# Kernel optimization log

Hardware: AMD Instinct MI355X
Metric: run time of the kernel (lower is better)

The kernel has to match this reference:

```python
import jax, jax.numpy as jnp
import numpy as np

ROPE_BASE = 10000.0

def _rope_tables(pos, d_head):
    # pos: (T,) int; returns cos,sin of shape (T, d_head//2)
    half = d_head // 2
    inv_freq = 1.0 / (ROPE_BASE ** (jnp.arange(half, dtype=jnp.float32) / half))
    ang = pos.astype(jnp.float32)[:, None] * inv_freq[None, :]
    return jnp.cos(ang), jnp.sin(ang)

def _apply_rope(x, cos, sin):
    # x: (B, H, T, D); cos/sin: (T, D//2); rotate-half convention
    x1, x2 = jnp.split(x, 2, axis=-1)
    c = cos[None, None, :, :]
    s = sin[None, None, :, :]
    return jnp.concatenate([x1 * c - x2 * s, x1 * s + x2 * c], axis=-1)

def setup_inputs() -> dict:
    key = jax.random.key(0)
    ks = jax.random.split(key, 8)
    B, T, C = 16, 4, 2048
    n_head, n_kv_head, d_head = 16, 4, 128
    S_cache = 4096
    sd = 1.0 / np.sqrt(C)
    return {
        "x": jax.random.normal(ks[0], (B, T, C), dtype=jnp.float32),
        "cache_k": jax.random.normal(ks[1], (B, n_kv_head, S_cache, d_head), dtype=jnp.float32),
        "cache_v": jax.random.normal(ks[2], (B, n_kv_head, S_cache, d_head), dtype=jnp.float32),
        "wq": jax.random.normal(ks[3], (C, n_head * d_head), dtype=jnp.float32) * sd,
        "wk": jax.random.normal(ks[4], (C, n_kv_head * d_head), dtype=jnp.float32) * sd,
        "wv": jax.random.normal(ks[5], (C, n_kv_head * d_head), dtype=jnp.float32) * sd,
        "w_proj": jax.random.normal(ks[6], (C, C), dtype=jnp.float32) * sd,
        "start_pos": 4096,
    }

def reference(x, cache_k, cache_v, wq, wk, wv, w_proj, start_pos):
    B, T, C = x.shape
    n_head, n_kv_head = 16, 4
    d_head = C // n_head
    group_size = n_head // n_kv_head
    sliding_window, sink = 2048, 4

    # projections -> (B, H, T, D)
    q = (x @ wq).reshape(B, T, n_head, d_head).transpose(0, 2, 1, 3)
    k = (x @ wk).reshape(B, T, n_kv_head, d_head).transpose(0, 2, 1, 3)
    v = (x @ wv).reshape(B, T, n_kv_head, d_head).transpose(0, 2, 1, 3)

    # RoPE at absolute positions [start_pos, start_pos+T)
    pos = jnp.arange(start_pos, start_pos + T)
    cos, sin = _rope_tables(pos, d_head)
    q = _apply_rope(q, cos, sin)
    k = _apply_rope(k, cos, sin)

    # KV cache concat along sequence dim
    k_all = jnp.concatenate([cache_k, k], axis=2)
    v_all = jnp.concatenate([cache_v, v], axis=2)

    # sliding window + attention sink slicing (4096+T > 2048+4)
    if k_all.shape[2] > sliding_window + sink:
        k_all = jnp.concatenate([k_all[:, :, :sink, :], k_all[:, :, -sliding_window:, :]], axis=2)
        v_all = jnp.concatenate([v_all[:, :, :sink, :], v_all[:, :, -sliding_window:, :]], axis=2)

    # GQA: expand KV heads to match query heads (repeat_interleave on head dim)
    k_attn = jnp.repeat(k_all, group_size, axis=1)
    v_attn = jnp.repeat(v_all, group_size, axis=1)

    # SDPA, is_causal=False (decode path with cache), dropout=0 (eval)
    scale = 1.0 / jnp.sqrt(jnp.float32(d_head))
    scores = jnp.einsum('bhtd,bhsd->bhts', q, k_attn) * scale
    attn = jax.nn.softmax(scores, axis=-1)
    y = jnp.einsum('bhts,bhsd->bhtd', attn, v_attn)

    y = y.transpose(0, 2, 1, 3).reshape(B, T, C)
    return y @ w_proj
```

## Files before the change

kernel.cpp:

```cpp
#include <hip/hip_runtime.h>
#include <math.h>

#define BB   16
#define TT   4
#define CC   2048
#define NH   16
#define NKV  4
#define DH   128
#define GRP  4
#define SCACHE 4096
#define SATT 2052
#define CS   128
#define NCH  17
#define KSPL 8

typedef unsigned int  uint32;
typedef unsigned short ushort_t;
typedef __attribute__((ext_vector_type(8))) __bf16 bf16x8;
typedef __attribute__((ext_vector_type(4))) float  f32x4;

__device__ __forceinline__ uint32 f2bf_bits(float f) {
    uint32 u = __float_as_uint(f);
    return (u + 0x7FFFu + ((u >> 16) & 1u)) >> 16;
}
__device__ __forceinline__ uint32 pk2(float lo, float hi) {
    return f2bf_bits(lo) | (f2bf_bits(hi) << 16);
}

#define Q_OFF    0
#define KNEW_OFF 524288
#define VNEW_OFF 655360
#define Y_OFF    786432
#define SCR_OFF  1310720

__global__ __launch_bounds__(256) void k_qkv(
    const float* __restrict__ x, const float* __restrict__ wq,
    const float* __restrict__ wk, const float* __restrict__ wv,
    float* __restrict__ part_qkv)
{
    __shared__ float xs[64][256];
    int ns = blockIdx.x, ks = blockIdx.y;
    int tid = threadIdx.x;
    int k0 = ks * 256;

    #pragma unroll
    for (int it = 0; it < 16; ++it) {
        int slot = it * 256 + tid;
        int row = slot >> 6, c4 = slot & 63;
        *(float4*)&xs[row][c4 * 4] = *(const float4*)(x + (size_t)row * CC + k0 + c4 * 4);
    }
    __syncthreads();

    int cp = tid & 31, rg = tid >> 5;
    const float* wp; int ldw, col;
    if (ns < 32)      { ldw = 2048; col = ns * 64 + cp * 2;
                        wp = wq + (size_t)k0 * 2048 + ns * 64 + cp * 2; }
    else if (ns < 40) { ldw = 512;  col = 2048 + (ns - 32) * 64 + cp * 2;
                        wp = wk + (size_t)k0 * 512 + (ns - 32) * 64 + cp * 2; }
    else              { ldw = 512;  col = 2560 + (ns - 40) * 64 + cp * 2;
                        wp = wv + (size_t)k0 * 512 + (ns - 40) * 64 + cp * 2; }

    float a[16];
    #pragma unroll
    for (int i = 0; i < 16; ++i) a[i] = 0.f;

    for (int k = 0; k < 256; k += 4) {
        float2 w0 = *(const float2*)(wp);
        float2 w1 = *(const float2*)(wp + ldw);
        float2 w2 = *(const float2*)(wp + 2 * ldw);
        float2 w3 = *(const float2*)(wp + 3 * ldw);
        wp += 4 * ldw;
        #pragma unroll
        for (int m = 0; m < 8; ++m) {
            float4 xv = *(const float4*)&xs[rg * 8 + m][k];
            float s0 = a[2*m], s1 = a[2*m+1];
            s0 = fmaf(xv.x, w0.x, s0); s1 = fmaf(xv.x, w0.y, s1);
            s0 = fmaf(xv.y, w1.x, s0); s1 = fmaf(xv.y, w1.y, s1);
            s0 = fmaf(xv.z, w2.x, s0); s1 = fmaf(xv.z, w2.y, s1);
            s0 = fmaf(xv.w, w3.x, s0); s1 = fmaf(xv.w, w3.y, s1);
            a[2*m] = s0; a[2*m+1] = s1;
        }
    }
    #pragma unroll
    for (int m = 0; m < 8; ++m)
        *(float2*)(part_qkv + ((size_t)(ks * 64 + rg * 8 + m) * 3072) + col) =
            make_float2(a[2*m], a[2*m+1]);
}

__global__ __launch_bounds__(256) void k_fix(
    const float* __restrict__ part_qkv, const int* __restrict__ spp,
    float* __restrict__ qws, float* __restrict__ knew, float* __restrict__ vnew)
{
    int u = blockIdx.x * 256 + threadIdx.x;
    int m = blockIdx.y;
    int b = m >> 2, t = m & 3;
    int sp = spp[0];
    const float NEG_L2_10K_64 = -0.20762050593048633f;

    if (u < 1024) {
        int h = u >> 6, d = u & 63;
        int col = h * 128 + d;
        float s1 = 0.f, s2 = 0.f;
        #pragma unroll
        for (int ks = 0; ks < KSPL; ++ks) {
            const float* p = part_qkv + (size_t)(ks * 64 + m) * 3072;
            s1 += p[col]; s2 += p[col + 64];
        }
        float inv = exp2f((float)d * NEG_L2_10K_64);
        float ang = (float)(sp + t) * inv;
        float cc = cosf(ang), ss = sinf(ang);
        float* dst = qws + (size_t)((b * NH + h) * TT + t) * DH + d;
        dst[0]  = s1 * cc - s2 * ss;
        dst[64] = s1 * ss + s2 * cc;
    } else if (u < 1280) {
        int v = u - 1024;
        int kv = v >> 6, d = v & 63;
        int col = 2048 + kv * 128 + d;
        float s1 = 0.f, s2 = 0.f;
        #pragma unroll
        for (int ks = 0; ks < KSPL; ++ks) {
            const float* p = part_qkv + (size_t)(ks * 64 + m) * 3072;
            s1 += p[col]; s2 += p[col + 64];
        }
        float inv = exp2f((float)d * NEG_L2_10K_64);
        float ang = (float)(sp + t) * inv;
        float cc = cosf(ang), ss = sinf(ang);
        float* dst = knew + (size_t)((b * NKV + kv) * TT + t) * DH + d;
        dst[0]  = s1 * cc - s2 * ss;
        dst[64] = s1 * ss + s2 * cc;
    } else {
        int v = u - 1280;
        int c0 = v * 2;
        int kv = c0 >> 7, dd = c0 & 127;
        float s1 = 0.f, s2 = 0.f;
        #pragma unroll
        for (int ks = 0; ks < KSPL; ++ks) {
            const float* p = part_qkv + (size_t)(ks * 64 + m) * 3072 + 2560 + c0;
            s1 += p[0]; s2 += p[1];
        }
        float* dst = vnew + (size_t)((b * NKV + kv) * TT + t) * DH + dd;
        dst[0] = s1; dst[1] = s2;
    }
}

__device__ __forceinline__ const float* kv_row(
    const float* cache, const float* newt, int bk, int j)
{
    if (j < 4)         return cache + ((size_t)bk * SCACHE + j) * DH;
    else if (j < 2048) return cache + ((size_t)bk * SCACHE + j + 2048) * DH;
    else               return newt  + ((size_t)(bk * TT + (j - 2048))) * DH;
}

__global__ __launch_bounds__(256) void k_attn(
    const float* __restrict__ qws,
    const float* __restrict__ kc, const float* __restrict__ vc,
    const float* __restrict__ knew, const float* __restrict__ vnew,
    float* __restrict__ part)
{
    __shared__ ushort_t kv_lds[128 * 136];
    __shared__ ushort_t p_lds[16 * 136];
    __shared__ float    red_a[64];
    __shared__ float    red_b[64];

    int bx = blockIdx.x;
    int c  = bx % NCH;
    int bk = bx / NCH;
    int b  = bk >> 2, kvh = bk & 3;
    int j0 = c * CS;
    int jn = (SATT - j0 < CS) ? (SATT - j0) : CS;
    int tid  = threadIdx.x;
    int wave = tid >> 6, lane = tid & 63;
    int quad = lane >> 4, l15 = lane & 15;
    const float scale = 0.08838834764831845f;

    bf16x8 aq[4];
    {
        int h = kvh * GRP + (l15 >> 2), t = l15 & 3;
        const float* qr = qws + (size_t)((b * NH + h) * TT + t) * DH;
        #pragma unroll
        for (int ks = 0; ks < 4; ++ks) {
            const float* s = qr + ks * 32 + quad * 8;
            float4 f0 = *(const float4*)s;
            float4 f1 = *(const float4*)(s + 4);
            union { uint32 u[4]; bf16x8 v; } pk;
            pk.u[0] = pk2(f0.x, f0.y); pk.u[1] = pk2(f0.z, f0.w);
            pk.u[2] = pk2(f1.x, f1.y); pk.u[3] = pk2(f1.z, f1.w);
            aq[ks] = pk.v;
        }
    }

    {
        float4 kf[16];
        #pragma unroll
        for (int it = 0; it < 8; ++it) {
            int slot = it * 256 + tid;
            int row = slot >> 4, d0 = (slot & 15) * 8;
            const float* kr = kv_row(kc, knew, bk, j0 + (row < jn ? row : 0)) + d0;
            kf[2*it]   = *(const float4*)kr;
            kf[2*it+1] = *(const float4*)(kr + 4);
        }
        #pragma unroll
        for (int it = 0; it < 8; ++it) {
            int slot = it * 256 + tid;
            int row = slot >> 4, d0 = (slot & 15) * 8;
            union { uint32 u[4]; bf16x8 v; } pk;
            pk.u[0] = pk.u[1] = pk.u[2] = pk.u[3] = 0;
            if (row < jn) {
                pk.u[0] = pk2(kf[2*it].x, kf[2*it].y);
                pk.u[1] = pk2(kf[2*it].z, kf[2*it].w);
                pk.u[2] = pk2(kf[2*it+1].x, kf[2*it+1].y);
                pk.u[3] = pk2(kf[2*it+1].z, kf[2*it+1].w);
            }
            *(bf16x8*)&kv_lds[row * 136 + d0] = pk.v;
        }
    }
    __syncthreads();

    int n0 = wave * 32;
    f32x4 s0 = {0.f, 0.f, 0.f, 0.f}, s1 = {0.f, 0.f, 0.f, 0.f};
    #pragma unroll
    for (int ks = 0; ks < 4; ++ks) {
        bf16x8 b0 = *(const bf16x8*)&kv_lds[(n0 + l15) * 136 + ks * 32 + quad * 8];
        bf16x8 b1 = *(const bf16x8*)&kv_lds[(n0 + 16 + l15) * 136 + ks * 32 + quad * 8];
        s0 = __builtin_amdgcn_mfma_f32_16x16x32_bf16(aq[ks], b0, s0, 0, 0, 0);
        s1 = __builtin_amdgcn_mfma_f32_16x16x32_bf16(aq[ks], b1, s1, 0, 0, 0);
    }

    float4 va[8], vb[8];
    int key0 = 2 * lane;
    bool okA = key0 < jn, okB = key0 + 1 < jn;
    {
        const float* ra = kv_row(vc, vnew, bk, j0 + (okA ? key0 : 0));
        const float* rb = kv_row(vc, vnew, bk, j0 + (okB ? key0 + 1 : 0));
        #pragma unroll
        for (int i = 0; i < 8; ++i) {
            int d = wave * 32 + i * 4;
            va[i] = *(const float4*)(ra + d);
            vb[i] = *(const float4*)(rb + d);
        }
    }

    int c0 = n0 + l15, c1 = n0 + 16 + l15;
    bool v0ok = c0 < jn, v1ok = c1 < jn;
    float sc0[4], sc1[4];
    #pragma unroll
    for (int i = 0; i < 4; ++i) {
        sc0[i] = v0ok ? s0[i] * scale : -1e30f;
        sc1[i] = v1ok ? s1[i] * scale : -1e30f;
        float v = fmaxf(sc0[i], sc1[i]);
        v = fmaxf(v, __shfl_xor(v, 1));
        v = fmaxf(v, __shfl_xor(v, 2));
        v = fmaxf(v, __shfl_xor(v, 4));
        v = fmaxf(v, __shfl_xor(v, 8));
        if (l15 == 0) red_a[wave * 16 + quad * 4 + i] = v;
    }
    __syncthreads();

    #pragma unroll
    for (int i = 0; i < 4; ++i) {
        int r = quad * 4 + i;
        float M = fmaxf(fmaxf(red_a[r], red_a[16 + r]),
                        fmaxf(red_a[32 + r], red_a[48 + r]));
        float p0 = __expf(sc0[i] - M);
        float p1 = __expf(sc1[i] - M);
        p_lds[r * 136 + c0] = (ushort_t)f2bf_bits(p0);
        p_lds[r * 136 + c1] = (ushort_t)f2bf_bits(p1);
        float v = p0 + p1;
        v += __shfl_xor(v, 1);
        v += __shfl_xor(v, 2);
        v += __shfl_xor(v, 4);
        v += __shfl_xor(v, 8);
        if (l15 == 0) red_b[wave * 16 + r] = v;
    }

    {
        uint32* vt32 = (uint32*)kv_lds;
        #pragma unroll
        for (int i = 0; i < 8; ++i) {
            int d = wave * 32 + i * 4;
            float4 fa = okA ? va[i] : make_float4(0.f, 0.f, 0.f, 0.f);
            float4 fb = okB ? vb[i] : make_float4(0.f, 0.f, 0.f, 0.f);
            vt32[(d + 0) * 68 + lane] = pk2(fa.x, fb.x);
            vt32[(d + 1) * 68 + lane] = pk2(fa.y, fb.y);
            vt32[(d + 2) * 68 + lane] = pk2(fa.z, fb.z);
            vt32[(d + 3) * 68 + lane] = pk2(fa.w, fb.w);
        }
    }
    __syncthreads();

    if (tid < 16) {
        int r = tid;
        float M = fmaxf(fmaxf(red_a[r], red_a[16 + r]),
                        fmaxf(red_a[32 + r], red_a[48 + r]));
        float L = red_b[r] + red_b[16 + r] + red_b[32 + r] + red_b[48 + r];
        float* rp = part + ((size_t)(bk * NCH + c) * 16 + r) * 132;
        rp[0] = M; rp[1] = L;
    }

    int d0 = wave * 32;
    f32x4 o0 = {0.f, 0.f, 0.f, 0.f}, o1 = {0.f, 0.f, 0.f, 0.f};
    #pragma unroll
    for (int ks = 0; ks < 4; ++ks) {
        bf16x8 ap = *(const bf16x8*)&p_lds[l15 * 136 + ks * 32 + quad * 8];
        bf16x8 b0 = *(const bf16x8*)&kv_lds[(d0 + l15) * 136 + ks * 32 + quad * 8];
        bf16x8 b1 = *(const bf16x8*)&kv_lds[(d0 + 16 + l15) * 136 + ks * 32 + quad * 8];
        o0 = __builtin_amdgcn_mfma_f32_16x16x32_bf16(ap, b0, o0, 0, 0, 0);
        o1 = __builtin_amdgcn_mfma_f32_16x16x32_bf16(ap, b1, o1, 0, 0, 0);
    }
    float* dstb = part + (size_t)(bk * NCH + c) * 16 * 132;
    #pragma unroll
    for (int i = 0; i < 4; ++i) {
        int row = quad * 4 + i;
        dstb[row * 132 + 4 + d0 + l15]      = o0[i];
        dstb[row * 132 + 4 + d0 + 16 + l15] = o1[i];
    }
}

__global__ __launch_bounds__(128) void k_comb(
    const float* __restrict__ part, float* __restrict__ yws)
{
    int bx = blockIdx.x;
    int t = bx & 3, h = (bx >> 2) & 15, b = bx >> 6;
    int bk = b * NKV + (h >> 2);
    int r  = (h & 3) * 4 + t;
    int d  = threadIdx.x;
    float M = -1e30f;
    for (int c = 0; c < NCH; ++c)
        M = fmaxf(M, part[((size_t)(bk * NCH + c) * 16 + r) * 132]);
    float L = 0.f, y = 0.f;
    for (int c = 0; c < NCH; ++c) {
        const float* pp = part + ((size_t)(bk * NCH + c) * 16 + r) * 132;
        float w = __expf(pp[0] - M);
        L += w * pp[1];
        y  = fmaf(w, pp[4 + d], y);
    }
    yws[(size_t)(b * TT + t) * CC + h * DH + d] = y / L;
}

__global__ __launch_bounds__(256) void k_proj(
    const float* __restrict__ yws, const float* __restrict__ wp,
    float* __restrict__ part_p)
{
    __shared__ float xs[64][256];
    int ns = blockIdx.x, ks = blockIdx.y;
    int tid = threadIdx.x;
    int k0 = ks * 256;
    #pragma unroll
    for (int it = 0; it < 16; ++it) {
        int slot = it * 256 + tid;
        int row = slot >> 6, c4 = slot & 63;
        *(float4*)&xs[row][c4 * 4] = *(const float4*)(yws + (size_t)row * CC + k0 + c4 * 4);
    }
    __syncthreads();

    int cp = tid & 31, rg = tid >> 5;
    int n = ns * 64 + cp * 2;
    const float* w = wp + (size_t)k0 * CC + n;
    float a[16];
    #pragma unroll
    for (int i = 0; i < 16; ++i) a[i] = 0.f;

    for (int k = 0; k < 256; k += 4) {
        float2 w0 = *(const float2*)(w);
        float2 w1 = *(const float2*)(w + CC);
        float2 w2 = *(const float2*)(w + 2 * CC);
        float2 w3 = *(const float2*)(w + 3 * CC);
        w += 4 * CC;
        #pragma unroll
        for (int m = 0; m < 8; ++m) {
            float4 xv = *(const float4*)&xs[rg * 8 + m][k];
            float s0 = a[2*m], s1 = a[2*m+1];
            s0 = fmaf(xv.x, w0.x, s0); s1 = fmaf(xv.x, w0.y, s1);
            s0 = fmaf(xv.y, w1.x, s0); s1 = fmaf(xv.y, w1.y, s1);
            s0 = fmaf(xv.z, w2.x, s0); s1 = fmaf(xv.z, w2.y, s1);
            s0 = fmaf(xv.w, w3.x, s0); s1 = fmaf(xv.w, w3.y, s1);
            a[2*m] = s0; a[2*m+1] = s1;
        }
    }
    #pragma unroll
    for (int m = 0; m < 8; ++m)
        *(float2*)(part_p + ((size_t)(ks * 64 + rg * 8 + m) * CC) + n) =
            make_float2(a[2*m], a[2*m+1]);
}

__global__ __launch_bounds__(256) void k_out(
    const float* __restrict__ part_p, float* __restrict__ out)
{
    int gt = blockIdx.x * 256 + threadIdx.x;
    float s = 0.f;
    #pragma unroll
    for (int ks = 0; ks < KSPL; ++ks) s += part_p[(size_t)ks * 64 * CC + gt];
    out[gt] = s;
}

extern "C" void kernel_launch(void* const* d_in, const int* in_sizes, int n_in,
                              void* d_out, int out_size, void* d_ws, size_t ws_size,
                              hipStream_t stream)
{
    const float* x   = (const float*)d_in[0];
    const float* ck  = (const float*)d_in[1];
    const float* cv  = (const float*)d_in[2];
    const float* wq  = (const float*)d_in[3];
    const float* wk  = (const float*)d_in[4];
    const float* wv  = (const float*)d_in[5];
    const float* wpj = (const float*)d_in[6];
    const int*   sp  = (const int*)d_in[7];
    char* ws = (char*)d_ws;
    float* qws  = (float*)(ws + Q_OFF);
    float* knew = (float*)(ws + KNEW_OFF);
    float* vnew = (float*)(ws + VNEW_OFF);
    float* yws  = (float*)(ws + Y_OFF);
    float* scr  = (float*)(ws + SCR_OFF);
    float* out  = (float*)d_out;

    hipLaunchKernelGGL(k_qkv,  dim3(48, 8),   dim3(256), 0, stream, x, wq, wk, wv, scr);
    hipLaunchKernelGGL(k_fix,  dim3(6, 64),   dim3(256), 0, stream, scr, sp, qws, knew, vnew);
    hipLaunchKernelGGL(k_attn, dim3(64 * NCH), dim3(256), 0, stream, qws, ck, cv, knew, vnew, scr);
    hipLaunchKernelGGL(k_comb, dim3(1024),    dim3(128), 0, stream, scr, yws);
    hipLaunchKernelGGL(k_proj, dim3(32, 8),   dim3(256), 0, stream, yws, wpj, scr);
    hipLaunchKernelGGL(k_out,  dim3(512),     dim3(256), 0, stream, scr, out);
}
```

Baseline: 361.7 us.

## Load K directly into MFMA registers, skip LDS staging, and prefetch V early

The attention kernel now loads each wave's K rows straight from global memory into registers in the MFMA B-operand layout. This removes the shared-memory staging pass for K and one block-wide barrier. V loads are issued at kernel start and split into two halves, so part of the V transpose into LDS overlaps the score MFMAs and softmax. This should cut latency and synchronisation in a memory-bound kernel, at the cost of more live registers and less regular K load patterns.

```diff
diff --git a/kernel.cpp b/kernel.cpp
--- a/kernel.cpp
+++ b/kernel.cpp
@@ -157,7 +157,7 @@
     const float* __restrict__ knew, const float* __restrict__ vnew,
     float* __restrict__ part)
 {
-    __shared__ ushort_t kv_lds[128 * 136];
+    __shared__ ushort_t vt_lds[128 * 136];
     __shared__ ushort_t p_lds[16 * 136];
     __shared__ float    red_a[64];
     __shared__ float    red_b[64];
@@ -173,6 +173,34 @@
     int quad = lane >> 4, l15 = lane & 15;
     const float scale = 0.08838834764831845f;
 
+    int n0 = wave * 32;
+
+    int rA = n0 + l15, rB = n0 + 16 + l15;
+    const float* kA = kv_row(kc, knew, bk, j0 + (rA < jn ? rA : 0));
+    const float* kB = kv_row(kc, knew, bk, j0 + (rB < jn ? rB : 0));
+    float4 ka[8], kb[8];
+    #pragma unroll
+    for (int ks = 0; ks < 4; ++ks) {
+        const float* pa = kA + ks * 32 + quad * 8;
+        const float* pb = kB + ks * 32 + quad * 8;
+        ka[2*ks]   = *(const float4*)pa;
+        ka[2*ks+1] = *(const float4*)(pa + 4);
+        kb[2*ks]   = *(const float4*)pb;
+        kb[2*ks+1] = *(const float4*)(pb + 4);
+    }
+
+    int key0 = 2 * lane;
+    bool okA = key0 < jn, okB = key0 + 1 < jn;
+    const float* rva = kv_row(vc, vnew, bk, j0 + (okA ? key0 : 0));
+    const float* rvb = kv_row(vc, vnew, bk, j0 + (okB ? key0 + 1 : 0));
+    float4 va0[4], vb0[4];
+    #pragma unroll
+    for (int i = 0; i < 4; ++i) {
+        int d = n0 + i * 4;
+        va0[i] = *(const float4*)(rva + d);
+        vb0[i] = *(const float4*)(rvb + d);
+    }
+
     bf16x8 aq[4];
     {
         int h = kvh * GRP + (l15 >> 2), t = l15 & 3;
@@ -189,55 +217,39 @@
         }
     }
 
-    {
-        float4 kf[16];
-        #pragma unroll
-        for (int it = 0; it < 8; ++it) {
-            int slot = it * 256 + tid;
-            int row = slot >> 4, d0 = (slot & 15) * 8;
-            const float* kr = kv_row(kc, knew, bk, j0 + (row < jn ? row : 0)) + d0;
-            kf[2*it]   = *(const float4*)kr;
-            kf[2*it+1] = *(const float4*)(kr + 4);
-        }
-        #pragma unroll
-        for (int it = 0; it < 8; ++it) {
-            int slot = it * 256 + tid;
-            int row = slot >> 4, d0 = (slot & 15) * 8;
-            union { uint32 u[4]; bf16x8 v; } pk;
-            pk.u[0] = pk.u[1] = pk.u[2] = pk.u[3] = 0;
-            if (row < jn) {
-                pk.u[0] = pk2(kf[2*it].x, kf[2*it].y);
-                pk.u[1] = pk2(kf[2*it].z, kf[2*it].w);
-                pk.u[2] = pk2(kf[2*it+1].x, kf[2*it+1].y);
-                pk.u[3] = pk2(kf[2*it+1].z, kf[2*it+1].w);
-            }
-            *(bf16x8*)&kv_lds[row * 136 + d0] = pk.v;
-        }
-    }
-    __syncthreads();
-
-    int n0 = wave * 32;
     f32x4 s0 = {0.f, 0.f, 0.f, 0.f}, s1 = {0.f, 0.f, 0.f, 0.f};
     #pragma unroll
     for (int ks = 0; ks < 4; ++ks) {
-        bf16x8 b0 = *(const bf16x8*)&kv_lds[(n0 + l15) * 136 + ks * 32 + quad * 8];
-        bf16x8 b1 = *(const bf16x8*)&kv_lds[(n0 + 16 + l15) * 136 + ks * 32 + quad * 8];
-        s0 = __builtin_amdgcn_mfma_f32_16x16x32_bf16(aq[ks], b0, s0, 0, 0, 0);
-        s1 = __builtin_amdgcn_mfma_f32_16x16x32_bf16(aq[ks], b1, s1, 0, 0, 0);
-    }
-
-    float4 va[8], vb[8];
-    int key0 = 2 * lane;
-    bool okA = key0 < jn, okB = key0 + 1 < jn;
-    {
-        const float* ra = kv_row(vc, vnew, bk, j0 + (okA ? key0 : 0));
-        const float* rb = kv_row(vc, vnew, bk, j0 + (okB ? key0 + 1 : 0));
-        #pragma unroll
-        for (int i = 0; i < 8; ++i) {
-            int d = wave * 32 + i * 4;
-            va[i] = *(const float4*)(ra + d);
-            vb[i] = *(const float4*)(rb + d);
-        }
+        union { uint32 u[4]; bf16x8 v; } pa, pb;
+        pa.u[0] = pk2(ka[2*ks].x,   ka[2*ks].y);
+        pa.u[1] = pk2(ka[2*ks].z,   ka[2*ks].w);
+        pa.u[2] = pk2(ka[2*ks+1].x, ka[2*ks+1].y);
+        pa.u[3] = pk2(ka[2*ks+1].z, ka[2*ks+1].w);
+        pb.u[0] = pk2(kb[2*ks].x,   kb[2*ks].y);
+        pb.u[1] = pk2(kb[2*ks].z,   kb[2*ks].w);
+        pb.u[2] = pk2(kb[2*ks+1].x, kb[2*ks+1].y);
+        pb.u[3] = pk2(kb[2*ks+1].z, kb[2*ks+1].w);
+        s0 = __builtin_amdgcn_mfma_f32_16x16x32_bf16(aq[ks], pa.v, s0, 0, 0, 0);
+        s1 = __builtin_amdgcn_mfma_f32_16x16x32_bf16(aq[ks], pb.v, s1, 0, 0, 0);
+    }
+
+    uint32* vt32 = (uint32*)vt_lds;
+    #pragma unroll
+    for (int i = 0; i < 4; ++i) {
+        int d = n0 + i * 4;
+        float4 fa = okA ? va0[i] : make_float4(0.f, 0.f, 0.f, 0.f);
+        float4 fb = okB ? vb0[i] : make_float4(0.f, 0.f, 0.f, 0.f);
+        vt32[(d + 0) * 68 + lane] = pk2(fa.x, fb.x);
+        vt32[(d + 1) * 68 + lane] = pk2(fa.y, fb.y);
+        vt32[(d + 2) * 68 + lane] = pk2(fa.z, fb.z);
+        vt32[(d + 3) * 68 + lane] = pk2(fa.w, fb.w);
+    }
+    float4 va1[4], vb1[4];
+    #pragma unroll
+    for (int i = 0; i < 4; ++i) {
+        int d = n0 + 16 + i * 4;
+        va1[i] = *(const float4*)(rva + d);
+        vb1[i] = *(const float4*)(rvb + d);
     }
 
     int c0 = n0 + l15, c1 = n0 + 16 + l15;
@@ -273,18 +285,15 @@
         if (l15 == 0) red_b[wave * 16 + r] = v;
     }
 
-    {
-        uint32* vt32 = (uint32*)kv_lds;
-        #pragma unroll
-        for (int i = 0; i < 8; ++i) {
-            int d = wave * 32 + i * 4;
-            float4 fa = okA ? va[i] : make_float4(0.f, 0.f, 0.f, 0.f);
-            float4 fb = okB ? vb[i] : make_float4(0.f, 0.f, 0.f, 0.f);
-            vt32[(d + 0) * 68 + lane] = pk2(fa.x, fb.x);
-            vt32[(d + 1) * 68 + lane] = pk2(fa.y, fb.y);
-            vt32[(d + 2) * 68 + lane] = pk2(fa.z, fb.z);
-            vt32[(d + 3) * 68 + lane] = pk2(fa.w, fb.w);
-        }
+    #pragma unroll
+    for (int i = 0; i < 4; ++i) {
+        int d = n0 + 16 + i * 4;
+        float4 fa = okA ? va1[i] : make_float4(0.f, 0.f, 0.f, 0.f);
+        float4 fb = okB ? vb1[i] : make_float4(0.f, 0.f, 0.f, 0.f);
+        vt32[(d + 0) * 68 + lane] = pk2(fa.x, fb.x);
+        vt32[(d + 1) * 68 + lane] = pk2(fa.y, fb.y);
+        vt32[(d + 2) * 68 + lane] = pk2(fa.z, fb.z);
+        vt32[(d + 3) * 68 + lane] = pk2(fa.w, fb.w);
     }
     __syncthreads();
 
@@ -302,8 +311,8 @@
     #pragma unroll
     for (int ks = 0; ks < 4; ++ks) {
         bf16x8 ap = *(const bf16x8*)&p_lds[l15 * 136 + ks * 32 + quad * 8];
-        bf16x8 b0 = *(const bf16x8*)&kv_lds[(d0 + l15) * 136 + ks * 32 + quad * 8];
-        bf16x8 b1 = *(const bf16x8*)&kv_lds[(d0 + 16 + l15) * 136 + ks * 32 + quad * 8];
+        bf16x8 b0 = *(const bf16x8*)&vt_lds[(d0 + l15) * 136 + ks * 32 + quad * 8];
+        bf16x8 b1 = *(const bf16x8*)&vt_lds[(d0 + 16 + l15) * 136 + ks * 32 + quad * 8];
         o0 = __builtin_amdgcn_mfma_f32_16x16x32_bf16(ap, b0, o0, 0, 0, 0);
         o1 = __builtin_amdgcn_mfma_f32_16x16x32_bf16(ap, b1, o1, 0, 0, 0);
     }
```

New measurement: 369.0 us. +2.0%, slower.
